# Kernel optimization log

Measured on AMD Instinct MI355X. Metric: run time of the kernel, lower is better.

The kernel has to match this reference:

```python
import jax, jax.numpy as jnp
import numpy as np
from jax import lax

HIDDEN = 16
DN = ('NCHW', 'OIHW', 'NCHW')

def setup_inputs() -> dict:
    key = jax.random.key(0)
    k1, k2, k3 = jax.random.split(key, 3)
    b, t, c, h, w = 8, 12, 5, 256, 256
    x = jax.random.normal(k1, (b, t, c, h, w), dtype=jnp.float32)
    # PyTorch-like init scale for conv weights
    W_cell = jax.random.normal(k2, (4 * HIDDEN, c + HIDDEN, 3, 3), dtype=jnp.float32) * 0.05
    b_cell = jnp.zeros((4 * HIDDEN,), dtype=jnp.float32)
    W_final = jax.random.normal(k3, (1, HIDDEN, 1, 1), dtype=jnp.float32) * 0.1
    b_final = jnp.zeros((1,), dtype=jnp.float32)
    return {"x": x, "W_cell": W_cell, "b_cell": b_cell,
            "W_final": W_final, "b_final": b_final}

def _cell_step(h_c, x_t, W_cell, b_cell):
    h_cur, c_cur = h_c
    combined = jnp.concatenate([x_t, h_cur], axis=1)          # [B, C+H, H, W]
    conv = lax.conv_general_dilated(combined, W_cell, (1, 1), 'SAME',
                                    dimension_numbers=DN)
    conv = conv + b_cell[None, :, None, None]                  # [B, 4H, H, W]
    cc_i, cc_f, cc_o, cc_g = jnp.split(conv, 4, axis=1)
    i = jax.nn.sigmoid(cc_i)
    f = jax.nn.sigmoid(cc_f)
    o = jax.nn.sigmoid(cc_o)
    g = jnp.tanh(cc_g)
    c_next = f * c_cur + i * g
    h_next = o * jnp.tanh(c_next)
    return h_next, c_next

def reference(x, W_cell, b_cell, W_final, b_final):
    b, t, c, hh, ww = x.shape
    h0 = jnp.zeros((b, HIDDEN, hh, ww), dtype=x.dtype)
    c0 = jnp.zeros((b, HIDDEN, hh, ww), dtype=x.dtype)
    xt = jnp.moveaxis(x, 1, 0)  # [T, B, C, H, W] for scan over time

    def step(carry, x_t):
        return _cell_step(carry, x_t, W_cell, b_cell), None

    (h_last, _), _ = lax.scan(step, (h0, c0), xt)
    out = lax.conv_general_dilated(h_last, W_final, (1, 1), 'SAME',
                                   dimension_numbers=DN)
    out = out + b_final[None, :, None, None]
    return out
```

## Files before the change

kernel.cpp:

```cpp
#include <hip/hip_runtime.h>
#include <math.h>

#define HIDDEN 16
#define CIN 5
#define BB 8
#define TT 12
#define HH 256
#define WW 256
#define TX 32
#define TY 8
#define HALO_X 34
#define HALO_Y 10
#define NPX (HALO_X * HALO_Y)
#define STRIDE 40
#define NBLK_PERSIST 1024
#define NTILES 2048
#define NRING 84
#define ROWSH 24
#define XSTEP (HH * WW * 8)

typedef __attribute__((ext_vector_type(8))) short bf16x8;
typedef __attribute__((ext_vector_type(4))) float floatx4;

__device__ __forceinline__ unsigned short f2bf(float f) {
    unsigned int u = __float_as_uint(f);
    u += 0x7fffu + ((u >> 16) & 1u);
    return (unsigned short)(u >> 16);
}
__device__ __forceinline__ float bf2f(unsigned short s) {
    return __uint_as_float(((unsigned int)s) << 16);
}
__device__ __forceinline__ float rcpf(float x) {
    float r;
    asm("v_rcp_f32 %0, %1" : "=v"(r) : "v"(x));
    return r;
}
__device__ __forceinline__ float fast_sigmoid(float x) {
    return rcpf(1.0f + __expf(-x));
}
__device__ __forceinline__ float fast_tanh(float x) {
    float e2 = __expf(-2.0f * fabsf(x));
    float t = (1.0f - e2) * rcpf(1.0f + e2);
    return copysignf(t, x);
}
__device__ __forceinline__ float leg_sigmoid(float x) { return 1.0f / (1.0f + __expf(-x)); }
__device__ __forceinline__ float leg_tanh(float x) {
    float e2 = __expf(-2.0f * fabsf(x));
    float t = (1.0f - e2) / (1.0f + e2);
    return copysignf(t, x);
}

__global__ void prep_w_kernel(const float* __restrict__ Wc,
                              unsigned short* __restrict__ Wfrag) {
    int i = blockIdx.x * 256 + threadIdx.x;
    if (i >= 9 * 4 * 64 * 8) return;
    int j    = i & 7;
    int lane = (i >> 3) & 63;
    int g    = (i >> 9) & 3;
    int tap  = i >> 11;
    int k    = ((lane >> 4) << 3) + j;
    int col  = lane & 15;
    int o    = g * 16 + col;
    float w  = 0.0f;
    if (k < 21) {
        int ci_ref = (k < 16) ? (5 + k) : (k - 16);
        w = Wc[(o * 21 + ci_ref) * 9 + tap];
    }
    Wfrag[i] = f2bf(w);
}

__global__ void prep_x_kernel(const float* __restrict__ x,
                              unsigned short* __restrict__ xp) {
    size_t n = (size_t)blockIdx.x * 256 + threadIdx.x;
    const size_t TOTPX = (size_t)BB * TT * HH * WW;
    if (n >= TOTPX) return;
    size_t bt  = n / (size_t)(HH * WW);
    size_t pix = n - bt * (size_t)(HH * WW);
    const float* src = x + bt * (size_t)CIN * HH * WW + pix;
    unsigned short v[8];
    #pragma unroll
    for (int c = 0; c < CIN; ++c) v[c] = f2bf(src[(size_t)c * HH * WW]);
    v[5] = 0; v[6] = 0; v[7] = 0;
    *(uint4*)&xp[n * 8] = *(const uint4*)v;
}

__global__ void prep_flags_kernel(unsigned int* __restrict__ flags) {
    int i = blockIdx.x * 256 + threadIdx.x;
    if (i < NTILES) flags[i] = 0;
}

__global__ __launch_bounds__(256, 4)
void convlstm_persistent_kernel(const float* __restrict__ x,
                                const unsigned short* __restrict__ xp,
                                unsigned short* __restrict__ ha,
                                unsigned short* __restrict__ hbuf,
                                const unsigned short* __restrict__ Wfrag,
                                const float* __restrict__ bias,
                                const float* __restrict__ Wf,
                                const float* __restrict__ bfin,
                                float* __restrict__ out,
                                unsigned int* __restrict__ flags,
                                int use_xp) {
    __shared__ unsigned short hx[2 * NPX * ROWSH + 8];
    const int ZOFF = 2 * NPX * ROWSH;

    const int tid  = threadIdx.x;
    const int lane = tid & 63;
    const int wave = tid >> 6;
    const int u    = lane & 15;
    const int quad = lane >> 4;
    const int bid  = (int)blockIdx.x;

    int ntile[2], x0v[2], y0v[2], bbv[2];
    #pragma unroll
    for (int tl = 0; tl < 2; ++tl) {
        int n = (bid & 7) * 256 + (bid >> 3) + tl * 128;
        ntile[tl] = n;
        x0v[tl] = (n & 7) * TX;
        y0v[tl] = ((n >> 3) & 31) * TY;
        bbv[tl] = n >> 8;
    }

    int nb_id[2];
    unsigned nb_act = 0;
    {
        int s  = lane + (lane >= 4 ? 1 : 0);
        int dy = s / 3 - 1;
        int dx = s - (s / 3) * 3 - 1;
        #pragma unroll
        for (int tl = 0; tl < 2; ++tl) {
            int n  = ntile[tl];
            int tx = n & 7;
            int ty = (n >> 3) & 31;
            bool act = (lane < 8) && (tx + dx >= 0) && (tx + dx < 8)
                                  && (ty + dy >= 0) && (ty + dy < 32);
            nb_id[tl] = act ? (n + dy * 8 + dx) : 0;
            if (act) nb_act |= 1u << tl;
        }
    }

    int xof[2][2];
    int pixv[2][2];
    unsigned inbm = 0;
    #pragma unroll
    for (int tl = 0; tl < 2; ++tl) {
        #pragma unroll
        for (int it = 0; it < 2; ++it) {
            int i  = tid + it * 256;
            int ly = i / HALO_X;
            int lx = i - ly * HALO_X;
            int gy = y0v[tl] + ly - 1;
            int gx = x0v[tl] + lx - 1;
            bool inb = (gy >= 0 && gy < HH && gx >= 0 && gx < WW) && (i < NPX);
            int pix = gy * WW + gx;
            pixv[tl][it] = pix;
            xof[tl][it]  = (bbv[tl] * TT * HH * WW + pix) * 8;
            if (inb) inbm |= 1u << (tl * 2 + it);
        }
    }

    int rrow = 0;
    int rgoff[2] = {0, 0};
    unsigned ringm = 0;
    if (tid < NRING) {
        int ly, lx;
        if (tid < 34)      { ly = 0;                lx = tid; }
        else if (tid < 68) { ly = HALO_Y - 1;       lx = tid - 34; }
        else { int k = tid - 68; ly = 1 + (k >> 1); lx = (k & 1) * (HALO_X - 1); }
        rrow = ly * HALO_X + lx;
        #pragma unroll
        for (int tl = 0; tl < 2; ++tl) {
            int gy = y0v[tl] + ly - 1;
            int gx = x0v[tl] + lx - 1;
            bool inb = (gy >= 0 && gy < HH && gx >= 0 && gx < WW);
            rgoff[tl] = (bbv[tl] * HH * WW + gy * WW + gx) * HIDDEN;
            if (inb) ringm |= 1u << tl;
        }
    }

    uint4 xr0 = {0, 0, 0, 0}, xr1 = {0, 0, 0, 0};
    if (use_xp) {
        if (inbm & 1u) xr0 = *(const uint4*)&xp[xof[0][0]];
        if (tid < NPX - 256 && (inbm & 2u)) xr1 = *(const uint4*)&xp[xof[0][1]];
    }

    for (int i = tid; i < 2 * NPX; i += 256) {
        uint4 z = {0, 0, 0, 0};
        *(uint4*)&hx[i * ROWSH]     = z;
        *(uint4*)&hx[i * ROWSH + 8] = z;
    }
    if (tid == 0) { uint4 z = {0, 0, 0, 0}; *(uint4*)&hx[ZOFF] = z; }

    float bg[4];
    #pragma unroll
    for (int g = 0; g < 4; ++g) bg[g] = bias[g * 16 + u];
    const float wfu = Wf[u];
    const float bf0 = bfin[0];
    const int msel  = (quad < 3) ? ROWSH : 0;

    float cA[2][2][4];
    float cB[2][2][4];
    #pragma unroll
    for (int a = 0; a < 2; ++a)
        #pragma unroll
        for (int m = 0; m < 2; ++m)
            #pragma unroll
            for (int r = 0; r < 4; ++r) { cA[a][m][r] = 0.0f; cB[a][m][r] = 0.0f; }

    #pragma unroll 1
    for (int t = 0; t < TT; ++t) {
        const unsigned short* h_in  = (t & 1) ? ha : hbuf;
        unsigned short*       h_out = (t & 1) ? hbuf : ha;
        const int first = (t == 0);
        const int last  = (t == TT - 1);

        #pragma unroll
        for (int tl = 0; tl < 2; ++tl) {
            const int n   = ntile[tl];
            const int x0  = x0v[tl];
            const int y0  = y0v[tl];
            const int bb  = bbv[tl];
            const int TLB = tl * NPX * ROWSH;

            if (t > 0) {
                if (wave == 0) {
                    const bool act = (nb_act >> tl) & 1;
                    const unsigned need = (unsigned)t;
                    for (;;) {
                        unsigned v = act
                            ? __hip_atomic_load(&flags[nb_id[tl]], __ATOMIC_RELAXED,
                                                __HIP_MEMORY_SCOPE_AGENT)
                            : 0xFFFFFFFFu;
                        if (__all(v >= need)) break;
                        __builtin_amdgcn_s_sleep(2);
                    }
                    if (tid == 0) __threadfence();
                }
                __syncthreads();
            }

            if (use_xp) {
                *(uint4*)&hx[TLB + tid * ROWSH + 16] = xr0;
                if (tid < NPX - 256)
                    *(uint4*)&hx[TLB + (tid + 256) * ROWSH + 16] = xr1;
            } else {
                #pragma unroll
                for (int it = 0; it < 2; ++it) {
                    if (it == 1 && tid >= NPX - 256) break;
                    const bool inb = (inbm >> (tl * 2 + it)) & 1;
                    unsigned short v[8];
                    #pragma unroll
                    for (int ci = 0; ci < CIN; ++ci) {
                        float f = 0.0f;
                        if (inb) f = x[(((size_t)bb * TT + t) * CIN + ci) * (size_t)(HH * WW)
                                       + pixv[tl][it]];
                        v[ci] = f2bf(f);
                    }
                    v[5] = 0; v[6] = 0; v[7] = 0;
                    *(uint4*)&hx[TLB + (tid + it * 256) * ROWSH + 16] = *(const uint4*)v;
                }
            }
            if (!first && tid < NRING && ((ringm >> tl) & 1)) {
                const unsigned short* hp = h_in + rgoff[tl];
                *(uint4*)&hx[TLB + rrow * ROWSH]     = *(const uint4*)&hp[0];
                *(uint4*)&hx[TLB + rrow * ROWSH + 8] = *(const uint4*)&hp[8];
            }
            if (use_xp) {
                const int ntl = tl ^ 1;
                const int nt  = t + tl;
                if (nt < TT) {
                    uint4 z4 = {0, 0, 0, 0};
                    xr0 = ((inbm >> (ntl * 2)) & 1)
                        ? *(const uint4*)&xp[xof[ntl][0] + nt * XSTEP] : z4;
                    if (tid < NPX - 256)
                        xr1 = ((inbm >> (ntl * 2 + 1)) & 1)
                            ? *(const uint4*)&xp[xof[ntl][1] + nt * XSTEP] : z4;
                }
            }
            __syncthreads();

            #pragma unroll 1
            for (int half = 0; half < 2; ++half) {
                floatx4 acc[2][4];
                int A[2];
                #pragma unroll
                for (int mh = 0; mh < 2; ++mh) {
                    int ml = half * 2 + mh;
                    int m  = wave + ml * 4;
                    int my = m >> 1;
                    int mx = (m & 1) << 4;
                    int bpx = my * HALO_X + mx + u;
                    A[mh] = (quad < 3) ? (TLB + bpx * ROWSH + quad * 8) : ZOFF;
                    #pragma unroll
                    for (int g = 0; g < 4; ++g)
                        acc[mh][g] = (floatx4){bg[g], bg[g], bg[g], bg[g]};
                }

                #pragma unroll 3
                for (int tap = 0; tap < 9; ++tap) {
                    int ky = tap / 3;
                    int kx = tap - ky * 3;
                    int ktap = ky * HALO_X + kx;
                    bf16x8 bfr[4];
                    #pragma unroll
                    for (int g = 0; g < 4; ++g)
                        bfr[g] = *(const bf16x8*)&Wfrag[(size_t)((tap * 4 + g) * 64 + lane) * 8];
                    #pragma unroll
                    for (int mh = 0; mh < 2; ++mh) {
                        bf16x8 af = *(const bf16x8*)&hx[A[mh] + ktap * msel];
                        #pragma unroll
                        for (int g = 0; g < 4; ++g)
                            acc[mh][g] = __builtin_amdgcn_mfma_f32_16x16x32_bf16(
                                af, bfr[g], acc[mh][g], 0, 0, 0);
                    }
                }

                #pragma unroll
                for (int mh = 0; mh < 2; ++mh) {
                    int ml = half * 2 + mh;
                    int m  = wave + ml * 4;
                    int my = m >> 1;
                    int mx = (m & 1) << 4;
                    int py = y0 + my;
                    int col0 = mx + quad * 4;
                    int erow = (my + 1) * HALO_X + col0 + 1;
                    int eaddr = TLB + erow * ROWSH + u;
                    size_t gidx0 = ((size_t)bb * HH * WW + (size_t)py * WW + x0 + col0)
                                   * HIDDEN + u;
                    bool topbot = (my == 0) || (my == TY - 1);
                    #pragma unroll
                    for (int r = 0; r < 4; ++r) {
                        float ig = fast_sigmoid(acc[mh][0][r]);
                        float fg = fast_sigmoid(acc[mh][1][r]);
                        float og = fast_sigmoid(acc[mh][2][r]);
                        float gg = fast_tanh(acc[mh][3][r]);
                        float c_old = half ? cB[tl][mh][r] : cA[tl][mh][r];
                        float c_new = fg * c_old + ig * gg;
                        if (half) cB[tl][mh][r] = c_new; else cA[tl][mh][r] = c_new;
                        float hval = og * fast_tanh(c_new);
                        if (last) {
                            float s = wfu * hval;
                            s += __shfl_xor(s, 1);
                            s += __shfl_xor(s, 2);
                            s += __shfl_xor(s, 4);
                            s += __shfl_xor(s, 8);
                            int col = col0 + r;
                            if (u == 0)
                                out[(size_t)bb * HH * WW + (size_t)py * WW + x0 + col]
                                    = s + bf0;
                        } else {
                            unsigned short hs = f2bf(hval);
                            hx[eaddr + r * ROWSH] = hs;
                            int col = col0 + r;
                            if (topbot || col == 0 || col == TX - 1)
                                h_out[gidx0 + (size_t)r * HIDDEN] = hs;
                        }
                    }
                }
            }

            if (!last) {
                __syncthreads();
                if (tid == 0) {
                    __threadfence();
                    __hip_atomic_store(&flags[n], (unsigned)(t + 1), __ATOMIC_RELAXED,
                                       __HIP_MEMORY_SCOPE_AGENT);
                }
            }
        }
    }
}

__global__ __launch_bounds__(256, 5)
void convlstm_step_kernel(const float* __restrict__ x, int t,
                          const unsigned short* __restrict__ xp,
                          const unsigned short* __restrict__ h_in,
                          unsigned short* __restrict__ h_out,
                          float* __restrict__ c_state,
                          const unsigned short* __restrict__ Wfrag,
                          const float* __restrict__ bias,
                          int first, int use_xp) {
    __shared__ unsigned short tile[NPX * STRIDE];

    const int tid  = threadIdx.x;
    const int lane = tid & 63;
    const int wave = tid >> 6;
    const int x0 = blockIdx.x * TX;
    const int y0 = blockIdx.y * TY;
    const int bb = blockIdx.z;

    for (int i = tid; i < NPX; i += 256) {
        int ly = i / HALO_X;
        int lx = i - ly * HALO_X;
        int gy = y0 + ly - 1;
        int gx = x0 + lx - 1;
        bool inb = (gy >= 0 && gy < HH && gx >= 0 && gx < WW);
        unsigned short* row = &tile[i * STRIDE];
        uint4 z = {0, 0, 0, 0};
        if (inb && !first) {
            size_t hbase = ((size_t)bb * HH * WW + (size_t)gy * WW + gx) * HIDDEN;
            *(uint4*)&row[0] = *(const uint4*)&h_in[hbase];
            *(uint4*)&row[8] = *(const uint4*)&h_in[hbase + 8];
        } else {
            *(uint4*)&row[0] = z;
            *(uint4*)&row[8] = z;
        }
        if (use_xp) {
            if (inb) {
                size_t xb = (((size_t)bb * TT + t) * (size_t)(HH * WW)
                             + (size_t)gy * WW + gx) * 8;
                *(uint4*)&row[16] = *(const uint4*)&xp[xb];
            } else {
                *(uint4*)&row[16] = z;
            }
        } else {
            #pragma unroll
            for (int ci = 0; ci < CIN; ++ci) {
                float v = 0.0f;
                if (inb) v = x[(((size_t)bb * TT + t) * CIN + ci) * (size_t)(HH * WW)
                               + (size_t)gy * WW + gx];
                row[16 + ci] = f2bf(v);
            }
            row[21] = 0; row[22] = 0; row[23] = 0;
        }
        *(uint4*)&row[24] = z;
    }
    __syncthreads();

    const int u    = lane & 15;
    const int quad = lane >> 4;

    float bg[4];
    #pragma unroll
    for (int g = 0; g < 4; ++g) bg[g] = bias[g * 16 + u];

    #pragma unroll 1
    for (int half = 0; half < 2; ++half) {
        floatx4 acc[2][4];
        int abase[2];
        #pragma unroll
        for (int mh = 0; mh < 2; ++mh) {
            int ml = half * 2 + mh;
            int m  = wave + ml * 4;
            int my = m >> 1;
            int mx = (m & 1) << 4;
            abase[mh] = (my * HALO_X + mx + u) * STRIDE + quad * 8;
            #pragma unroll
            for (int g = 0; g < 4; ++g)
                acc[mh][g] = (floatx4){bg[g], bg[g], bg[g], bg[g]};
        }

        #pragma unroll 3
        for (int tap = 0; tap < 9; ++tap) {
            int ky = tap / 3;
            int kx = tap - ky * 3;
            int toff = (ky * HALO_X + kx) * STRIDE;
            bf16x8 bfr[4];
            #pragma unroll
            for (int g = 0; g < 4; ++g)
                bfr[g] = *(const bf16x8*)&Wfrag[(size_t)((tap * 4 + g) * 64 + lane) * 8];
            #pragma unroll
            for (int mh = 0; mh < 2; ++mh) {
                bf16x8 af = *(const bf16x8*)&tile[abase[mh] + toff];
                #pragma unroll
                for (int g = 0; g < 4; ++g)
                    acc[mh][g] = __builtin_amdgcn_mfma_f32_16x16x32_bf16(
                        af, bfr[g], acc[mh][g], 0, 0, 0);
            }
        }

        #pragma unroll
        for (int mh = 0; mh < 2; ++mh) {
            int ml = half * 2 + mh;
            int m  = wave + ml * 4;
            int my = m >> 1;
            int mx = (m & 1) << 4;
            int py = y0 + my;
            #pragma unroll
            for (int r = 0; r < 4; ++r) {
                int pxx = x0 + mx + quad * 4 + r;
                size_t idx = ((size_t)bb * HH * WW + (size_t)py * WW + pxx) * HIDDEN + u;
                float ig = leg_sigmoid(acc[mh][0][r]);
                float fg = leg_sigmoid(acc[mh][1][r]);
                float og = leg_sigmoid(acc[mh][2][r]);
                float gg = leg_tanh(acc[mh][3][r]);
                float c_old = first ? 0.0f : c_state[idx];
                float c_new = fg * c_old + ig * gg;
                c_state[idx] = c_new;
                h_out[idx] = f2bf(og * leg_tanh(c_new));
            }
        }
    }
}

__global__ void final_conv_kernel(const unsigned short* __restrict__ h,
                                  const float* __restrict__ Wf,
                                  const float* __restrict__ bf_,
                                  float* __restrict__ out) {
    int i = blockIdx.x * 256 + threadIdx.x;
    if (i >= BB * HH * WW) return;
    size_t base = (size_t)i * HIDDEN;
    uint4 v0 = *(const uint4*)&h[base];
    uint4 v1 = *(const uint4*)&h[base + 8];
    const unsigned short* p0 = (const unsigned short*)&v0;
    const unsigned short* p1 = (const unsigned short*)&v1;
    float s = bf_[0];
    #pragma unroll
    for (int k = 0; k < 8; ++k) s += Wf[k] * bf2f(p0[k]);
    #pragma unroll
    for (int k = 0; k < 8; ++k) s += Wf[8 + k] * bf2f(p1[k]);
    out[i] = s;
}

extern "C" void kernel_launch(void* const* d_in, const int* in_sizes, int n_in,
                              void* d_out, int out_size, void* d_ws, size_t ws_size,
                              hipStream_t stream) {
    const float* x  = (const float*)d_in[0];
    const float* Wc = (const float*)d_in[1];
    const float* bc = (const float*)d_in[2];
    const float* Wf = (const float*)d_in[3];
    const float* bf = (const float*)d_in[4];
    float* out = (float*)d_out;

    char* ws = (char*)d_ws;
    const size_t h_bytes = (size_t)BB * HH * WW * HIDDEN * 2;
    const size_t c_bytes = (size_t)BB * HH * WW * HIDDEN * 4;
    const size_t w_bytes = 9 * 4 * 64 * 8 * 2;
    const size_t f_bytes = (size_t)NTILES * 4;
    const size_t x_bytes = (size_t)BB * TT * HH * WW * 8 * 2;

    unsigned short* h_a = (unsigned short*)(ws);
    unsigned short* h_b = (unsigned short*)(ws + h_bytes);
    float* c            = (float*)(ws + 2 * h_bytes);
    unsigned short* Wfr = (unsigned short*)(ws + 2 * h_bytes + c_bytes);
    unsigned int* flags = (unsigned int*)(ws + 2 * h_bytes + c_bytes + w_bytes);
    unsigned short* xp  = (unsigned short*)(ws + 2 * h_bytes + c_bytes + w_bytes + f_bytes);

    const int use_xp =
        (ws_size >= 2 * h_bytes + c_bytes + w_bytes + f_bytes + x_bytes) ? 1 : 0;

    prep_w_kernel<<<(9 * 4 * 64 * 8 + 255) / 256, 256, 0, stream>>>(Wc, Wfr);
    prep_flags_kernel<<<(NTILES + 255) / 256, 256, 0, stream>>>(flags);
    if (use_xp) {
        size_t totpx = (size_t)BB * TT * HH * WW;
        prep_x_kernel<<<(int)((totpx + 255) / 256), 256, 0, stream>>>(x, xp);
    }

    int occ = 0;
    hipOccupancyMaxActiveBlocksPerMultiprocessor(&occ, convlstm_persistent_kernel,
                                                 256, 0);
    bool done = false;
    if (occ >= 4) {
        const unsigned short* xp_arg = use_xp ? xp : (const unsigned short*)0;
        int use_xp_arg = use_xp;
        void* kargs[] = {
            (void*)&x, (void*)&xp_arg, (void*)&h_a, (void*)&h_b,
            (void*)&Wfr, (void*)&bc, (void*)&Wf, (void*)&bf,
            (void*)&out, (void*)&flags, (void*)&use_xp_arg
        };
        if (hipLaunchCooperativeKernel((const void*)convlstm_persistent_kernel,
                                       dim3(NBLK_PERSIST, 1, 1), dim3(256, 1, 1),
                                       kargs, 0, stream) == hipSuccess)
            done = true;
    }

    if (!done) {
        dim3 grid(WW / TX, HH / TY, BB);
        dim3 block(256, 1, 1);
        const unsigned short* h_in = h_a;
        for (int t = 0; t < TT; ++t) {
            unsigned short* h_out = (t & 1) ? h_b : h_a;
            convlstm_step_kernel<<<grid, block, 0, stream>>>(
                x, t, use_xp ? xp : (const unsigned short*)0,
                h_in, h_out, c, Wfr, bc, (t == 0) ? 1 : 0, use_xp);
            h_in = h_out;
        }
        final_conv_kernel<<<(BB * HH * WW + 255) / 256, 256, 0, stream>>>(
            h_in, Wf, bf, out);
    }
}
```

Measured before the change: 688.7 us.

## Merge two 32x8 tiles per block into one 64x8 persistent tile

Each persistent block now owns a single 64x8 spatial tile instead of two interleaved 32x8 tiles. Halo overhead shrinks, so fewer halo pixels are loaded, and the neighbour flag waits and barriers drop from two per timestep to one. The cost is that the one-tile-ahead x prefetch overlap between the two sub-tiles is lost, and dependency chains are coarser, with 1024 flags instead of 2048.

```diff
diff --git a/kernel.cpp b/kernel.cpp
--- a/kernel.cpp
+++ b/kernel.cpp
@@ -13,10 +13,15 @@
 #define HALO_Y 10
 #define NPX (HALO_X * HALO_Y)
 #define STRIDE 40
+#define PTX 64
+#define PTY 8
+#define PHX 66
+#define PHY 10
+#define PNPX (PHX * PHY)
+#define PRING 148
+#define ROWSH 24
+#define ZOFFP (PNPX * ROWSH)
 #define NBLK_PERSIST 1024
-#define NTILES 2048
-#define NRING 84
-#define ROWSH 24
 #define XSTEP (HH * WW * 8)
 
 typedef __attribute__((ext_vector_type(8))) short bf16x8;
@@ -86,7 +91,7 @@
 
 __global__ void prep_flags_kernel(unsigned int* __restrict__ flags) {
     int i = blockIdx.x * 256 + threadIdx.x;
-    if (i < NTILES) flags[i] = 0;
+    if (i < NBLK_PERSIST) flags[i] = 0;
 }
 
 __global__ __launch_bounds__(256, 4)
@@ -101,8 +106,7 @@
                                 float* __restrict__ out,
                                 unsigned int* __restrict__ flags,
                                 int use_xp) {
-    __shared__ unsigned short hx[2 * NPX * ROWSH + 8];
-    const int ZOFF = 2 * NPX * ROWSH;
+    __shared__ unsigned short hx[PNPX * ROWSH + 8];
 
     const int tid  = threadIdx.x;
     const int lane = tid & 63;
@@ -111,101 +115,87 @@
     const int quad = lane >> 4;
     const int bid  = (int)blockIdx.x;
 
-    int ntile[2], x0v[2], y0v[2], bbv[2];
-    #pragma unroll
-    for (int tl = 0; tl < 2; ++tl) {
-        int n = (bid & 7) * 256 + (bid >> 3) + tl * 128;
-        ntile[tl] = n;
-        x0v[tl] = (n & 7) * TX;
-        y0v[tl] = ((n >> 3) & 31) * TY;
-        bbv[tl] = n >> 8;
-    }
-
-    int nb_id[2];
-    unsigned nb_act = 0;
+    const int tile_id = (bid & 7) * 128 + (bid >> 3);
+    const int tq  = tile_id & 127;
+    const int tqx = tq & 3;
+    const int tqy = tq >> 2;
+    const int x0  = tqx * PTX;
+    const int y0  = tqy * PTY;
+    const int bb  = tile_id >> 7;
+
+    int nb_id = 0;
+    bool nb_act = false;
     {
         int s  = lane + (lane >= 4 ? 1 : 0);
         int dy = s / 3 - 1;
         int dx = s - (s / 3) * 3 - 1;
-        #pragma unroll
-        for (int tl = 0; tl < 2; ++tl) {
-            int n  = ntile[tl];
-            int tx = n & 7;
-            int ty = (n >> 3) & 31;
-            bool act = (lane < 8) && (tx + dx >= 0) && (tx + dx < 8)
-                                  && (ty + dy >= 0) && (ty + dy < 32);
-            nb_id[tl] = act ? (n + dy * 8 + dx) : 0;
-            if (act) nb_act |= 1u << tl;
-        }
-    }
-
-    int xof[2][2];
-    int pixv[2][2];
+        nb_act = (lane < 8) && (tqx + dx >= 0) && (tqx + dx < 4)
+                            && (tqy + dy >= 0) && (tqy + dy < 32);
+        nb_id = nb_act ? (tile_id + dy * 4 + dx) : 0;
+    }
+
+    int xof0 = 0, xof1 = 0, xof2 = 0;
+    int pix0 = 0, pix1 = 0, pix2 = 0;
     unsigned inbm = 0;
     #pragma unroll
-    for (int tl = 0; tl < 2; ++tl) {
-        #pragma unroll
-        for (int it = 0; it < 2; ++it) {
-            int i  = tid + it * 256;
-            int ly = i / HALO_X;
-            int lx = i - ly * HALO_X;
-            int gy = y0v[tl] + ly - 1;
-            int gx = x0v[tl] + lx - 1;
-            bool inb = (gy >= 0 && gy < HH && gx >= 0 && gx < WW) && (i < NPX);
-            int pix = gy * WW + gx;
-            pixv[tl][it] = pix;
-            xof[tl][it]  = (bbv[tl] * TT * HH * WW + pix) * 8;
-            if (inb) inbm |= 1u << (tl * 2 + it);
-        }
-    }
-
-    int rrow = 0;
-    int rgoff[2] = {0, 0};
-    unsigned ringm = 0;
-    if (tid < NRING) {
+    for (int it = 0; it < 3; ++it) {
+        int i = tid + it * 256;
+        if (it == 2 && tid >= PNPX - 512) break;
+        int ly = i / PHX;
+        int lx = i - ly * PHX;
+        int gy = y0 + ly - 1;
+        int gx = x0 + lx - 1;
+        bool inb = (gy >= 0 && gy < HH && gx >= 0 && gx < WW);
+        int pix = gy * WW + gx;
+        int xo  = (bb * TT * HH * WW + pix) * 8;
+        if (it == 0) { xof0 = xo; pix0 = pix; }
+        else if (it == 1) { xof1 = xo; pix1 = pix; }
+        else { xof2 = xo; pix2 = pix; }
+        if (inb) inbm |= 1u << it;
+    }
+
+    int rrow = 0, rgoff = 0;
+    bool ring_inb = false;
+    if (tid < PRING) {
         int ly, lx;
-        if (tid < 34)      { ly = 0;                lx = tid; }
-        else if (tid < 68) { ly = HALO_Y - 1;       lx = tid - 34; }
-        else { int k = tid - 68; ly = 1 + (k >> 1); lx = (k & 1) * (HALO_X - 1); }
-        rrow = ly * HALO_X + lx;
-        #pragma unroll
-        for (int tl = 0; tl < 2; ++tl) {
-            int gy = y0v[tl] + ly - 1;
-            int gx = x0v[tl] + lx - 1;
-            bool inb = (gy >= 0 && gy < HH && gx >= 0 && gx < WW);
-            rgoff[tl] = (bbv[tl] * HH * WW + gy * WW + gx) * HIDDEN;
-            if (inb) ringm |= 1u << tl;
-        }
-    }
-
-    uint4 xr0 = {0, 0, 0, 0}, xr1 = {0, 0, 0, 0};
+        if (tid < 66)       { ly = 0;              lx = tid; }
+        else if (tid < 132) { ly = PHY - 1;        lx = tid - 66; }
+        else { int k = tid - 132; ly = 1 + (k >> 1); lx = (k & 1) * (PHX - 1); }
+        rrow = ly * PHX + lx;
+        int gy = y0 + ly - 1;
+        int gx = x0 + lx - 1;
+        ring_inb = (gy >= 0 && gy < HH && gx >= 0 && gx < WW);
+        rgoff = (bb * HH * WW + gy * WW + gx) * HIDDEN;
+    }
+
+    uint4 xr0 = {0, 0, 0, 0}, xr1 = {0, 0, 0, 0}, xr2 = {0, 0, 0, 0};
     if (use_xp) {
-        if (inbm & 1u) xr0 = *(const uint4*)&xp[xof[0][0]];
-        if (tid < NPX - 256 && (inbm & 2u)) xr1 = *(const uint4*)&xp[xof[0][1]];
-    }
-
-    for (int i = tid; i < 2 * NPX; i += 256) {
+        if (inbm & 1u) xr0 = *(const uint4*)&xp[xof0];
+        if (inbm & 2u) xr1 = *(const uint4*)&xp[xof1];
+        if (tid < PNPX - 512 && (inbm & 4u)) xr2 = *(const uint4*)&xp[xof2];
+    }
+
+    for (int i = tid; i < PNPX; i += 256) {
         uint4 z = {0, 0, 0, 0};
         *(uint4*)&hx[i * ROWSH]     = z;
         *(uint4*)&hx[i * ROWSH + 8] = z;
     }
-    if (tid == 0) { uint4 z = {0, 0, 0, 0}; *(uint4*)&hx[ZOFF] = z; }
+    if (tid == 0) { uint4 z = {0, 0, 0, 0}; *(uint4*)&hx[ZOFFP] = z; }
 
     float bg[4];
     #pragma unroll
     for (int g = 0; g < 4; ++g) bg[g] = bias[g * 16 + u];
     const float wfu = Wf[u];
     const float bf0 = bfin[0];
-    const int msel  = (quad < 3) ? ROWSH : 0;
-
-    float cA[2][2][4];
-    float cB[2][2][4];
-    #pragma unroll
-    for (int a = 0; a < 2; ++a)
+
+    float cQ0[2][4], cQ1[2][4], cQ2[2][4], cQ3[2][4];
+    #pragma unroll
+    for (int m = 0; m < 2; ++m)
         #pragma unroll
-        for (int m = 0; m < 2; ++m)
-            #pragma unroll
-            for (int r = 0; r < 4; ++r) { cA[a][m][r] = 0.0f; cB[a][m][r] = 0.0f; }
+        for (int r = 0; r < 4; ++r) {
+            cQ0[m][r] = 0.0f; cQ1[m][r] = 0.0f;
+            cQ2[m][r] = 0.0f; cQ3[m][r] = 0.0f;
+        }
 
     #pragma unroll 1
     for (int t = 0; t < TT; ++t) {
@@ -214,93 +204,84 @@
         const int first = (t == 0);
         const int last  = (t == TT - 1);
 
-        #pragma unroll
-        for (int tl = 0; tl < 2; ++tl) {
-            const int n   = ntile[tl];
-            const int x0  = x0v[tl];
-            const int y0  = y0v[tl];
-            const int bb  = bbv[tl];
-            const int TLB = tl * NPX * ROWSH;
-
-            if (t > 0) {
-                if (wave == 0) {
-                    const bool act = (nb_act >> tl) & 1;
-                    const unsigned need = (unsigned)t;
-                    for (;;) {
-                        unsigned v = act
-                            ? __hip_atomic_load(&flags[nb_id[tl]], __ATOMIC_RELAXED,
-                                                __HIP_MEMORY_SCOPE_AGENT)
-                            : 0xFFFFFFFFu;
-                        if (__all(v >= need)) break;
-                        __builtin_amdgcn_s_sleep(2);
-                    }
-                    if (tid == 0) __threadfence();
+        if (t > 0) {
+            if (wave == 0) {
+                const unsigned need = (unsigned)t;
+                for (;;) {
+                    unsigned v = nb_act
+                        ? __hip_atomic_load(&flags[nb_id], __ATOMIC_RELAXED,
+                                            __HIP_MEMORY_SCOPE_AGENT)
+                        : 0xFFFFFFFFu;
+                    if (__all(v >= need)) break;
+                    __builtin_amdgcn_s_sleep(2);
                 }
-                __syncthreads();
-            }
-
-            if (use_xp) {
-                *(uint4*)&hx[TLB + tid * ROWSH + 16] = xr0;
-                if (tid < NPX - 256)
-                    *(uint4*)&hx[TLB + (tid + 256) * ROWSH + 16] = xr1;
-            } else {
+                if (tid == 0) __threadfence();
+            }
+            __syncthreads();
+        }
+
+        if (use_xp) {
+            *(uint4*)&hx[tid * ROWSH + 16]         = xr0;
+            *(uint4*)&hx[(tid + 256) * ROWSH + 16] = xr1;
+            if (tid < PNPX - 512)
+                *(uint4*)&hx[(tid + 512) * ROWSH + 16] = xr2;
+        } else {
+            #pragma unroll
+            for (int it = 0; it < 3; ++it) {
+                if (it == 2 && tid >= PNPX - 512) break;
+                int pv = (it == 0) ? pix0 : (it == 1) ? pix1 : pix2;
+                const bool inb = (inbm >> it) & 1;
+                unsigned short v[8];
                 #pragma unroll
-                for (int it = 0; it < 2; ++it) {
-                    if (it == 1 && tid >= NPX - 256) break;
-                    const bool inb = (inbm >> (tl * 2 + it)) & 1;
-                    unsigned short v[8];
-                    #pragma unroll
-                    for (int ci = 0; ci < CIN; ++ci) {
-                        float f = 0.0f;
-                        if (inb) f = x[(((size_t)bb * TT + t) * CIN + ci) * (size_t)(HH * WW)
-                                       + pixv[tl][it]];
-                        v[ci] = f2bf(f);
-                    }
-                    v[5] = 0; v[6] = 0; v[7] = 0;
-                    *(uint4*)&hx[TLB + (tid + it * 256) * ROWSH + 16] = *(const uint4*)v;
+                for (int ci = 0; ci < CIN; ++ci) {
+                    float f = 0.0f;
+                    if (inb) f = x[(((size_t)bb * TT + t) * CIN + ci) * (size_t)(HH * WW)
+                                   + pv];
+                    v[ci] = f2bf(f);
                 }
-            }
-            if (!first && tid < NRING && ((ringm >> tl) & 1)) {
-                const unsigned short* hp = h_in + rgoff[tl];
-                *(uint4*)&hx[TLB + rrow * ROWSH]     = *(const uint4*)&hp[0];
-                *(uint4*)&hx[TLB + rrow * ROWSH + 8] = *(const uint4*)&hp[8];
-            }
-            if (use_xp) {
-                const int ntl = tl ^ 1;
-                const int nt  = t + tl;
-                if (nt < TT) {
-                    uint4 z4 = {0, 0, 0, 0};
-                    xr0 = ((inbm >> (ntl * 2)) & 1)
-                        ? *(const uint4*)&xp[xof[ntl][0] + nt * XSTEP] : z4;
-                    if (tid < NPX - 256)
-                        xr1 = ((inbm >> (ntl * 2 + 1)) & 1)
-                            ? *(const uint4*)&xp[xof[ntl][1] + nt * XSTEP] : z4;
-                }
-            }
-            __syncthreads();
-
+                v[5] = 0; v[6] = 0; v[7] = 0;
+                *(uint4*)&hx[(tid + it * 256) * ROWSH + 16] = *(const uint4*)v;
+            }
+        }
+        if (!first && tid < PRING && ring_inb) {
+            const unsigned short* hp = h_in + rgoff;
+            *(uint4*)&hx[rrow * ROWSH]     = *(const uint4*)&hp[0];
+            *(uint4*)&hx[rrow * ROWSH + 8] = *(const uint4*)&hp[8];
+        }
+        if (use_xp && t + 1 < TT) {
+            uint4 z4 = {0, 0, 0, 0};
+            int ts = (t + 1) * XSTEP;
+            xr0 = (inbm & 1u) ? *(const uint4*)&xp[xof0 + ts] : z4;
+            xr1 = (inbm & 2u) ? *(const uint4*)&xp[xof1 + ts] : z4;
+            if (tid < PNPX - 512)
+                xr2 = (inbm & 4u) ? *(const uint4*)&xp[xof2 + ts] : z4;
+        }
+        __syncthreads();
+
+        #pragma unroll 1
+        for (int h1 = 0; h1 < 2; ++h1) {
             #pragma unroll 1
-            for (int half = 0; half < 2; ++half) {
+            for (int h2 = 0; h2 < 2; ++h2) {
+                const int qq = h1 * 2 + h2;
                 floatx4 acc[2][4];
                 int A[2];
                 #pragma unroll
                 for (int mh = 0; mh < 2; ++mh) {
-                    int ml = half * 2 + mh;
-                    int m  = wave + ml * 4;
-                    int my = m >> 1;
-                    int mx = (m & 1) << 4;
-                    int bpx = my * HALO_X + mx + u;
-                    A[mh] = (quad < 3) ? (TLB + bpx * ROWSH + quad * 8) : ZOFF;
+                    int my = qq * 2 + mh;
+                    int mx = wave << 4;
+                    int bpx = my * PHX + mx + u;
+                    A[mh] = (quad < 3) ? (bpx * ROWSH + quad * 8) : ZOFFP;
                     #pragma unroll
                     for (int g = 0; g < 4; ++g)
                         acc[mh][g] = (floatx4){bg[g], bg[g], bg[g], bg[g]};
                 }
+                const int msel = (quad < 3) ? ROWSH : 0;
 
                 #pragma unroll 3
                 for (int tap = 0; tap < 9; ++tap) {
                     int ky = tap / 3;
                     int kx = tap - ky * 3;
-                    int ktap = ky * HALO_X + kx;
+                    int ktap = ky * PHX + kx;
                     bf16x8 bfr[4];
                     #pragma unroll
                     for (int g = 0; g < 4; ++g)
@@ -317,26 +298,24 @@
 
                 #pragma unroll
                 for (int mh = 0; mh < 2; ++mh) {
-                    int ml = half * 2 + mh;
-                    int m  = wave + ml * 4;
-                    int my = m >> 1;
-                    int mx = (m & 1) << 4;
+                    int my = qq * 2 + mh;
                     int py = y0 + my;
-                    int col0 = mx + quad * 4;
-                    int erow = (my + 1) * HALO_X + col0 + 1;
-                    int eaddr = TLB + erow * ROWSH + u;
+                    int col0 = (wave << 4) + quad * 4;
+                    int eaddr = ((my + 1) * PHX + col0 + 1) * ROWSH + u;
                     size_t gidx0 = ((size_t)bb * HH * WW + (size_t)py * WW + x0 + col0)
                                    * HIDDEN + u;
-                    bool topbot = (my == 0) || (my == TY - 1);
+                    bool topbot = (my == 0) || (my == PTY - 1);
                     #pragma unroll
                     for (int r = 0; r < 4; ++r) {
                         float ig = fast_sigmoid(acc[mh][0][r]);
                         float fg = fast_sigmoid(acc[mh][1][r]);
                         float og = fast_sigmoid(acc[mh][2][r]);
                         float gg = fast_tanh(acc[mh][3][r]);
-                        float c_old = half ? cB[tl][mh][r] : cA[tl][mh][r];
+                        float c_old = h1 ? (h2 ? cQ3[mh][r] : cQ2[mh][r])
+                                         : (h2 ? cQ1[mh][r] : cQ0[mh][r]);
                         float c_new = fg * c_old + ig * gg;
-                        if (half) cB[tl][mh][r] = c_new; else cA[tl][mh][r] = c_new;
+                        if (h1) { if (h2) cQ3[mh][r] = c_new; else cQ2[mh][r] = c_new; }
+                        else    { if (h2) cQ1[mh][r] = c_new; else cQ0[mh][r] = c_new; }
                         float hval = og * fast_tanh(c_new);
                         if (last) {
                             float s = wfu * hval;
@@ -344,28 +323,27 @@
                             s += __shfl_xor(s, 2);
                             s += __shfl_xor(s, 4);
                             s += __shfl_xor(s, 8);
-                            int col = col0 + r;
                             if (u == 0)
-                                out[(size_t)bb * HH * WW + (size_t)py * WW + x0 + col]
+                                out[(size_t)bb * HH * WW + (size_t)py * WW + x0 + col0 + r]
                                     = s + bf0;
                         } else {
                             unsigned short hs = f2bf(hval);
                             hx[eaddr + r * ROWSH] = hs;
                             int col = col0 + r;
-                            if (topbot || col == 0 || col == TX - 1)
+                            if (topbot || col == 0 || col == PTX - 1)
                                 h_out[gidx0 + (size_t)r * HIDDEN] = hs;
                         }
                     }
                 }
             }
-
-            if (!last) {
-                __syncthreads();
-                if (tid == 0) {
-                    __threadfence();
-                    __hip_atomic_store(&flags[n], (unsigned)(t + 1), __ATOMIC_RELAXED,
-                                       __HIP_MEMORY_SCOPE_AGENT);
-                }
+        }
+
+        if (!last) {
+            __syncthreads();
+            if (tid == 0) {
+                __threadfence();
+                __hip_atomic_store(&flags[tile_id], (unsigned)(t + 1), __ATOMIC_RELAXED,
+                                   __HIP_MEMORY_SCOPE_AGENT);
             }
         }
     }
@@ -526,7 +504,7 @@
     const size_t h_bytes = (size_t)BB * HH * WW * HIDDEN * 2;
     const size_t c_bytes = (size_t)BB * HH * WW * HIDDEN * 4;
     const size_t w_bytes = 9 * 4 * 64 * 8 * 2;
-    const size_t f_bytes = (size_t)NTILES * 4;
+    const size_t f_bytes = (size_t)NBLK_PERSIST * 4;
     const size_t x_bytes = (size_t)BB * TT * HH * WW * 8 * 2;
 
     unsigned short* h_a = (unsigned short*)(ws);
@@ -540,7 +518,7 @@
         (ws_size >= 2 * h_bytes + c_bytes + w_bytes + f_bytes + x_bytes) ? 1 : 0;
 
     prep_w_kernel<<<(9 * 4 * 64 * 8 + 255) / 256, 256, 0, stream>>>(Wc, Wfr);
-    prep_flags_kernel<<<(NTILES + 255) / 256, 256, 0, stream>>>(flags);
+    prep_flags_kernel<<<(NBLK_PERSIST + 255) / 256, 256, 0, stream>>>(flags);
     if (use_xp) {
         size_t totpx = (size_t)BB * TT * HH * WW;
         prep_x_kernel<<<(int)((totpx + 255) / 256), 256, 0, stream>>>(x, xp);
```

After: 691.0 us. Within noise of the previous version (+0.3%).
